# Optimization experiments

Hardware: AMD Instinct MI355X
Metric: run time of the kernel (lower is better)

The kernel has to match this reference:

```python
import jax, jax.numpy as jnp
import numpy as np

T, D, H, B = 2048, 1152, 16, 8
DH = D // H  # 72


def _apply_rope(x, cos_h, sin_h):
    # x: [T, H, DH]; cos_h, sin_h: [T, DH//2] (already chunked halves)
    c = jnp.concatenate([cos_h, cos_h], axis=-1)[:, None, :]  # [T,1,DH]
    s = jnp.concatenate([sin_h, sin_h], axis=-1)[:, None, :]
    x1, x2 = jnp.split(x, 2, axis=-1)
    rot = jnp.concatenate([-x2, x1], axis=-1)
    return x * c + rot * s


def setup_inputs() -> dict:
    key = jax.random.key(0)
    ks = jax.random.split(key, 12)
    hidden_states = jax.random.normal(ks[0], (T, D), jnp.float32)
    inner = jnp.sort(jax.random.randint(ks[1], (B - 1,), 1, T))
    cu_seqlens = jnp.concatenate(
        [jnp.zeros((1,), jnp.int32), inner.astype(jnp.int32), jnp.full((1,), T, jnp.int32)])
    cos = jax.random.uniform(ks[2], (T, DH), jnp.float32, -1.0, 1.0)
    sin = jax.random.uniform(ks[3], (T, DH), jnp.float32, -1.0, 1.0)
    std = 0.02
    Wq = jax.random.normal(ks[4], (D, D), jnp.float32) * std
    Wk = jax.random.normal(ks[5], (D, D), jnp.float32) * std
    Wv = jax.random.normal(ks[6], (D, D), jnp.float32) * std
    Wo = jax.random.normal(ks[7], (D, D), jnp.float32) * std
    bq = jnp.zeros((D,), jnp.float32)
    bk = jnp.zeros((D,), jnp.float32)
    bv = jnp.zeros((D,), jnp.float32)
    bo = jnp.zeros((D,), jnp.float32)
    return {"hidden_states": hidden_states, "cu_seqlens": cu_seqlens,
            "cos": cos, "sin": sin,
            "Wq": Wq, "bq": bq, "Wk": Wk, "bk": bk,
            "Wv": Wv, "bv": bv, "Wo": Wo, "bo": bo}


def reference(hidden_states, cu_seqlens, cos, sin, Wq, bq, Wk, bk, Wv, bv, Wo, bo):
    t = hidden_states.shape[0]
    scale = DH ** -0.5
    q = (hidden_states @ Wq.T + bq).reshape(t, H, DH)
    k = (hidden_states @ Wk.T + bk).reshape(t, H, DH)
    v = (hidden_states @ Wv.T + bv).reshape(t, H, DH)
    # RoPE: cos/sin [T, DH] are chunked in half along last dim, first half used
    cos_h = cos[:, : DH // 2]
    sin_h = sin[:, : DH // 2]
    q = _apply_rope(q, cos_h, sin_h)
    k = _apply_rope(k, cos_h, sin_h)
    # segment ids from cu_seqlens -> block-diagonal (varlen) attention mask
    pos = jnp.arange(t)
    seg = jnp.searchsorted(cu_seqlens, pos, side='right') - 1  # [T]
    mask = seg[:, None] == seg[None, :]  # [T, T]
    scores = jnp.einsum('thd,shd->hts', q, k) * scale  # [H, T, T]
    scores = jnp.where(mask[None], scores, jnp.float32(-1e30))
    attn = jax.nn.softmax(scores, axis=-1)
    out = jnp.einsum('hts,shd->thd', attn, v).reshape(t, D)
    return out @ Wo.T + bo
```

## Files before the change

kernel.cpp:

```cpp
#include <hip/hip_runtime.h>

#define TT 2048
#define DM 1152
#define NHEAD 16
#define HDIM 72
#define HDP 96
#define HDV 80
#define KSPLIT 2

typedef __attribute__((ext_vector_type(8))) __bf16 bf16x8;
typedef __attribute__((ext_vector_type(4))) float f32x4;
typedef unsigned short u16;
typedef unsigned int u32;

__device__ inline u16 f2bf(float f){
  u32 u = __builtin_bit_cast(u32, f);
  return (u16)((u + 0x7FFFu + ((u >> 16) & 1u)) >> 16);
}
__device__ inline float bf2f(u16 v){
  return __builtin_bit_cast(float, ((u32)v) << 16);
}
__device__ inline bf16x8 ldb8(const u16* p){
  uint4 u = *(const uint4*)p;
  return __builtin_bit_cast(bf16x8, u);
}
__device__ inline f32x4 mfma16(bf16x8 a, bf16x8 b, f32x4 c){
  return __builtin_amdgcn_mfma_f32_16x16x32_bf16(a, b, c, 0, 0, 0);
}
__device__ inline void gload_lds16(const u16* g, u16* l){
  __builtin_amdgcn_global_load_lds(
      (const __attribute__((address_space(1))) void*)g,
      (__attribute__((address_space(3))) void*)l, 16, 0, 0);
}

__global__ void k_convert(const float* hid, const float* wq, const float* wk,
                          const float* wv, const float* wo, const int* cu,
                          u16* hb, u16* wqb, u16* wkb, u16* wvb, u16* wob,
                          u16* qhb, u16* khb, int* seg)
{
  long i = (long)blockIdx.x * blockDim.x + threadIdx.x;
  const long NHID = (long)TT * DM;
  const long NW = (long)DM * DM;
  const long NCV = NHID + 4*NW;
  if (i < NHID) {
    hb[i] = f2bf(hid[i]);
  } else if (i < NCV) {
    long j = i - NHID;
    int w = (int)(j / NW);
    long o = j - (long)w * NW;
    const float* src = (w==0)?wq:(w==1)?wk:(w==2)?wv:wo;
    u16* dst = (w==0)?wqb:(w==1)?wkb:(w==2)?wvb:wob;
    dst[o] = f2bf(src[o]);
  } else {
    long j = i - NCV;
    const long PER = (long)NHEAD*TT*12;
    int arr = (int)(j / PER);
    long r = j - (long)arr*PER;
    long th = r / 12;
    int c = (int)(r - th*12);
    ((u32*)(arr ? khb : qhb))[th*48 + 36 + c] = 0u;
  }
  if (i < TT) {
    int c = 0;
    for (int e = 0; e < 9; ++e) c += (cu[e] <= (int)i);
    seg[i] = c - 1;
  }
}

__device__ __forceinline__ void gemm128_body(const u16* __restrict__ A,
                                             const u16* __restrict__ W,
                                             const float* __restrict__ bias,
                                             void* out, int mode, float oscale)
{
  __shared__ __align__(16) u16 As[128*32];
  __shared__ __align__(16) u16 Bs[128*32];
  int tid = threadIdx.x;
  int lane = tid & 63, wid = tid >> 6;
  int l15 = lane & 15, quad = lane >> 4;
  int bm = blockIdx.x * 128, bn = blockIdx.y * 128;
  int wm = (wid>>1)*64, wn = (wid&1)*64;
  f32x4 acc[4][4] = {};
  const u16* ga = A + (long)(bm + (tid>>2))*DM + (tid&3)*8;
  const u16* gb = W + (long)(bn + (tid>>2))*DM + (tid&3)*8;
  u16* lA = As + wid*512;
  u16* lB = Bs + wid*512;
  for (int k0 = 0; k0 < DM; k0 += 32) {
    gload_lds16(ga + k0,          lA);
    gload_lds16(ga + k0 + 64*DM,  lA + 2048);
    gload_lds16(gb + k0,          lB);
    gload_lds16(gb + k0 + 64*DM,  lB + 2048);
    __syncthreads();
    bf16x8 af[4], bfr[4];
    for (int i=0;i<4;i++) af[i]  = ldb8(As + (wm + i*16 + l15)*32 + quad*8);
    for (int i=0;i<4;i++) bfr[i] = ldb8(Bs + (wn + i*16 + l15)*32 + quad*8);
    for (int mi=0;mi<4;mi++)
      for (int ni=0;ni<4;ni++)
        acc[mi][ni] = mfma16(af[mi], bfr[ni], acc[mi][ni]);
    __syncthreads();
  }
  for (int ni=0;ni<4;ni++){
    int n = bn + wn + ni*16 + l15;
    float bv_ = bias[n];
    int h = n / HDIM, dh = n - (n / HDIM)*HDIM;
    for (int mi=0;mi<4;mi++){
      int m0 = bm + wm + mi*16 + quad*4;
      for (int r=0;r<4;r++){
        float v = (acc[mi][ni][r] + bv_) * oscale;
        int m = m0 + r;
        if (mode == 0) {
          ((u16*)out)[((long)(h*TT + m))*HDP + dh] = f2bf(v);
        } else {
          ((u16*)out)[((long)(h*HDV + dh))*TT + m] = f2bf(v);
        }
      }
    }
  }
}

__global__ __launch_bounds__(256) void k_gemm_qkv(const u16* __restrict__ A,
    const u16* __restrict__ Wq, const u16* __restrict__ Wk, const u16* __restrict__ Wv,
    const float* __restrict__ bq, const float* __restrict__ bk, const float* __restrict__ bv,
    u16* oq, u16* ok, u16* ov)
{
  const float scale = 0.11785113019775793f;
  int z = blockIdx.z;
  if (z == 0)      gemm128_body(A, Wq, bq, oq, 0, scale);
  else if (z == 1) gemm128_body(A, Wk, bk, ok, 0, 1.0f);
  else             gemm128_body(A, Wv, bv, ov, 2, 1.0f);
}

__global__ __launch_bounds__(256) void k_gemm_o(const u16* __restrict__ A,
    const u16* __restrict__ W, const float* __restrict__ bias, float* out)
{
  __shared__ __align__(16) u16 As[64*32];
  __shared__ __align__(16) u16 Bs[128*32];
  int tid = threadIdx.x;
  int lane = tid & 63, wid = tid >> 6;
  int l15 = lane & 15, quad = lane >> 4;
  int bm = blockIdx.x * 64, bn = blockIdx.y * 128;
  int wm = (wid>>1)*32, wn = (wid&1)*64;
  f32x4 acc[2][4] = {};
  const u16* ga = A + (long)(bm + (tid>>2))*DM + (tid&3)*8;
  const u16* gb = W + (long)(bn + (tid>>2))*DM + (tid&3)*8;
  u16* lA = As + wid*512;
  u16* lB = Bs + wid*512;
  for (int k0 = 0; k0 < DM; k0 += 32) {
    gload_lds16(ga + k0,          lA);
    gload_lds16(gb + k0,          lB);
    gload_lds16(gb + k0 + 64*DM,  lB + 2048);
    __syncthreads();
    bf16x8 af[2], bfr[4];
    for (int i=0;i<2;i++) af[i]  = ldb8(As + (wm + i*16 + l15)*32 + quad*8);
    for (int i=0;i<4;i++) bfr[i] = ldb8(Bs + (wn + i*16 + l15)*32 + quad*8);
    for (int mi=0;mi<2;mi++)
      for (int ni=0;ni<4;ni++)
        acc[mi][ni] = mfma16(af[mi], bfr[ni], acc[mi][ni]);
    __syncthreads();
  }
  for (int ni=0;ni<4;ni++){
    int n = bn + wn + ni*16 + l15;
    float bv_ = bias[n];
    for (int mi=0;mi<2;mi++){
      int m0 = bm + wm + mi*16 + quad*4;
      for (int r=0;r<4;r++)
        out[(long)(m0 + r)*DM + n] = acc[mi][ni][r] + bv_;
    }
  }
}

__global__ void k_rope(u16* qh, u16* kh, const float* __restrict__ cosb,
                       const float* __restrict__ sinb)
{
  int i = blockIdx.x * blockDim.x + threadIdx.x;
  const int total = 2 * NHEAD * TT * 36;
  if (i >= total) return;
  int d = i % 36; int rest = i / 36;
  int t = rest % TT; rest /= TT;
  int h = rest % NHEAD; int qk = rest / NHEAD;
  u16* base = (qk ? kh : qh) + ((long)h*TT + t)*HDP;
  float x1 = bf2f(base[d]), x2 = bf2f(base[d+36]);
  float c = cosb[t*HDIM + d], s = sinb[t*HDIM + d];
  base[d]    = f2bf(x1*c - x2*s);
  base[d+36] = f2bf(x2*c + x1*s);
}

__global__ __launch_bounds__(256) void k_attn(const u16* __restrict__ qh,
                                              const u16* __restrict__ kh,
                                              const u16* __restrict__ vT,
                                              const int* __restrict__ seg,
                                              const int* __restrict__ cu,
                                              float* __restrict__ pacc,
                                              float* __restrict__ plsum)
{
  __shared__ __align__(16) u16 Ks[2][64*96];
  __shared__ __align__(16) u16 pbuf[4][16][72];
  int h = blockIdx.y;
  int z = blockIdx.z;
  int tid = threadIdx.x, lane = tid & 63, wid = tid >> 6;
  int l15 = lane & 15, quad = lane >> 4;
  int qb0 = blockIdx.x * 64;
  int qbase = qb0 + wid*16;

  const u16* qp = qh + ((long)h*TT + qbase + l15)*HDP + quad*8;
  bf16x8 qf0 = ldb8(qp), qf1 = ldb8(qp+32), qf2 = ldb8(qp+64);
  int segq[4];
  for (int r=0;r<4;r++) segq[r] = seg[qbase + quad*4 + r];
  f32x4 acc[5] = {};
  float lsum[4] = {0.f, 0.f, 0.f, 0.f};

  int seg_lo = seg[qb0], seg_hi = seg[qb0 + 63];
  int s_begin = cu[seg_lo] & ~63;
  int s_end = cu[seg_hi + 1];
  int nt = (s_end - s_begin + 63) >> 6;
  int nt0 = (nt + 1) >> 1;
  int it_lo = z ? nt0 : 0;
  int it_hi = z ? nt : nt0;

  const u16* kbase = kh + (long)h*TT*HDP;

  if (it_lo < it_hi) {
    {
      const u16* gk = kbase + (long)(s_begin + it_lo*64)*HDP + tid*8;
      u16* lK = Ks[0] + wid*512;
      gload_lds16(gk,        lK);
      gload_lds16(gk + 2048, lK + 2048);
      gload_lds16(gk + 4096, lK + 4096);
    }
    for (int it = it_lo; it < it_hi; ++it) {
      int s0 = s_begin + it*64;
      int cur = (it - it_lo) & 1;
      __syncthreads();
      if (it + 1 < it_hi) {
        const u16* gk = kbase + (long)(s0 + 64)*HDP + tid*8;
        u16* lK = Ks[cur^1] + wid*512;
        gload_lds16(gk,        lK);
        gload_lds16(gk + 2048, lK + 2048);
        gload_lds16(gk + 4096, lK + 4096);
      }
      f32x4 sc[4] = {};
      for (int j=0;j<4;j++){
        const u16* kp = Ks[cur] + (j*16 + l15)*96 + quad*8;
        sc[j] = mfma16(qf0, ldb8(kp),    sc[j]);
        sc[j] = mfma16(qf1, ldb8(kp+32), sc[j]);
        sc[j] = mfma16(qf2, ldb8(kp+64), sc[j]);
      }
      int sg[4];
      for (int j=0;j<4;j++) sg[j] = seg[s0 + j*16 + l15];
      float p[4][4];
      for (int j=0;j<4;j++)
        for (int r=0;r<4;r++){
          p[j][r] = (sg[j] == segq[r]) ? __expf(sc[j][r]) : 0.f;
          lsum[r] += p[j][r];
        }
      for (int j=0;j<4;j++)
        for (int r=0;r<4;r++)
          pbuf[wid][quad*4+r][j*16+l15] = f2bf(p[j][r]);
      bf16x8 pf0 = ldb8(&pbuf[wid][l15][quad*8]);
      bf16x8 pf1 = ldb8(&pbuf[wid][l15][32 + quad*8]);
      const u16* vp = vT + ((long)h*HDV + l15)*TT + s0 + quad*8;
      for (int n=0;n<5;n++){
        bf16x8 vf0 = ldb8(vp + (long)n*16*TT);
        bf16x8 vf1 = ldb8(vp + (long)n*16*TT + 32);
        acc[n] = mfma16(pf0, vf0, acc[n]);
        acc[n] = mfma16(pf1, vf1, acc[n]);
      }
    }
  }
  for (int off=1; off<16; off<<=1)
    for (int r=0;r<4;r++)
      lsum[r] += __shfl_xor(lsum[r], off, 64);
  for (int n=0;n<5;n++){
    int dh = n*16 + l15;
    for (int r=0;r<4;r++){
      int t = qbase + quad*4 + r;
      pacc[(((long)z*TT + t)*NHEAD + h)*HDV + dh] = acc[n][r];
    }
  }
  if (l15 == 0){
    for (int r=0;r<4;r++){
      int t = qbase + quad*4 + r;
      plsum[((long)z*TT + t)*NHEAD + h] = lsum[r];
    }
  }
}

__global__ void k_combine(const float* __restrict__ pacc,
                          const float* __restrict__ plsum,
                          u16* __restrict__ ao)
{
  int i = blockIdx.x*blockDim.x + threadIdx.x;
  const int total = TT*NHEAD*HDIM;
  if (i >= total) return;
  int dh = i % HDIM; int rest = i / HDIM;
  int h = rest % NHEAD; int t = rest / NHEAD;
  long i0 = ((long)t*NHEAD + h)*HDV + dh;
  float a = pacc[i0] + pacc[(long)TT*NHEAD*HDV + i0];
  float l = plsum[t*NHEAD + h] + plsum[TT*NHEAD + t*NHEAD + h];
  ao[(long)t*DM + h*HDIM + dh] = f2bf(a / l);
}

extern "C" void kernel_launch(void* const* d_in, const int* in_sizes, int n_in,
                              void* d_out, int out_size, void* d_ws, size_t ws_size,
                              hipStream_t stream)
{
  const float* hid  = (const float*)d_in[0];
  const int*   cu   = (const int*)d_in[1];
  const float* cosb = (const float*)d_in[2];
  const float* sinb = (const float*)d_in[3];
  const float* wq   = (const float*)d_in[4];
  const float* bq   = (const float*)d_in[5];
  const float* wk   = (const float*)d_in[6];
  const float* bk   = (const float*)d_in[7];
  const float* wv   = (const float*)d_in[8];
  const float* bv   = (const float*)d_in[9];
  const float* wo   = (const float*)d_in[10];
  const float* bo   = (const float*)d_in[11];

  char* ws = (char*)d_ws;
  u16* hb  = (u16*)ws; ws += (long)TT*DM*2;
  u16* wqb = (u16*)ws; ws += (long)DM*DM*2;
  u16* wkb = (u16*)ws; ws += (long)DM*DM*2;
  u16* wvb = (u16*)ws; ws += (long)DM*DM*2;
  u16* wob = (u16*)ws; ws += (long)DM*DM*2;
  u16* qhb = (u16*)ws; ws += (long)NHEAD*TT*HDP*2;
  u16* khb = (u16*)ws; ws += (long)NHEAD*TT*HDP*2;
  u16* vTb = (u16*)ws; ws += (long)NHEAD*HDV*TT*2;
  u16* aob = (u16*)ws; ws += (long)TT*DM*2;
  int* seg = (int*)ws; ws += (long)TT*4;
  float* pacc  = (float*)ws; ws += (long)KSPLIT*TT*NHEAD*HDV*4;
  float* plsum = (float*)ws; ws += (long)KSPLIT*TT*NHEAD*4;

  long nconv = (long)TT*DM + 4L*DM*DM + 2L*NHEAD*TT*12;
  k_convert<<<dim3((nconv + 255)/256), 256, 0, stream>>>(
      hid, wq, wk, wv, wo, cu, hb, wqb, wkb, wvb, wob, qhb, khb, seg);

  dim3 gqkv(TT/128, DM/128, 3);
  k_gemm_qkv<<<gqkv, 256, 0, stream>>>(hb, wqb, wkb, wvb, bq, bk, bv, qhb, khb, vTb);

  int nrope = 2*NHEAD*TT*36;
  k_rope<<<dim3((nrope + 255)/256), 256, 0, stream>>>(qhb, khb, cosb, sinb);

  dim3 ga(TT/64, NHEAD, KSPLIT);
  k_attn<<<ga, 256, 0, stream>>>(qhb, khb, vTb, seg, cu, pacc, plsum);

  int ncomb = TT*NHEAD*HDIM;
  k_combine<<<dim3((ncomb + 255)/256), 256, 0, stream>>>(pacc, plsum, aob);

  dim3 go(TT/64, DM/128);
  k_gemm_o<<<go, 256, 0, stream>>>(aob, wob, bo, (float*)d_out);
}
```

Before: 205.4 us.

## Double-buffer GEMMs with smaller tiles, vectorize conversion, range-based attention mask

The QKV and output-projection GEMMs now use double-buffered LDS with a single barrier per k-step. Their N tile is halved to 64, which roughly doubles the block count and improves occupancy on the many CUs, and launch bounds request 4 blocks per CU. The fp32-to-bf16 conversion kernel is vectorized to handle four elements per thread. The attention mask now compares key indices against per-row segment bounds instead of loading segment ids for every key tile. Smaller tiles lower per-block data reuse and raise the total number of global loads.

```diff
diff --git a/kernel.cpp b/kernel.cpp
--- a/kernel.cpp
+++ b/kernel.cpp
@@ -12,6 +12,7 @@
 typedef __attribute__((ext_vector_type(4))) float f32x4;
 typedef unsigned short u16;
 typedef unsigned int u32;
+typedef __attribute__((ext_vector_type(4))) u16 u16x4;
 
 __device__ inline u16 f2bf(float f){
   u32 u = __builtin_bit_cast(u32, f);
@@ -39,26 +40,32 @@
                           u16* qhb, u16* khb, int* seg)
 {
   long i = (long)blockIdx.x * blockDim.x + threadIdx.x;
-  const long NHID = (long)TT * DM;
-  const long NW = (long)DM * DM;
-  const long NCV = NHID + 4*NW;
-  if (i < NHID) {
-    hb[i] = f2bf(hid[i]);
-  } else if (i < NCV) {
-    long j = i - NHID;
-    int w = (int)(j / NW);
-    long o = j - (long)w * NW;
-    const float* src = (w==0)?wq:(w==1)?wk:(w==2)?wv:wo;
-    u16* dst = (w==0)?wqb:(w==1)?wkb:(w==2)?wvb:wob;
-    dst[o] = f2bf(src[o]);
+  const long NHID4 = (long)TT * DM / 4;
+  const long NW4 = (long)DM * DM / 4;
+  const long NC4 = NHID4 + 4*NW4;
+  if (i < NC4) {
+    const float4* src; u16* dst; long o;
+    if (i < NHID4) { src = (const float4*)hid; dst = hb; o = i; }
+    else {
+      long j = i - NHID4;
+      int w = (int)(j / NW4);
+      o = j - (long)w * NW4;
+      src = (const float4*)((w==0)?wq:(w==1)?wk:(w==2)?wv:wo);
+      dst = (w==0)?wqb:(w==1)?wkb:(w==2)?wvb:wob;
+    }
+    float4 v = src[o];
+    u16x4 r; r.x = f2bf(v.x); r.y = f2bf(v.y); r.z = f2bf(v.z); r.w = f2bf(v.w);
+    *(u16x4*)(dst + o*4) = r;
   } else {
-    long j = i - NCV;
+    long j = i - NC4;
     const long PER = (long)NHEAD*TT*12;
-    int arr = (int)(j / PER);
-    long r = j - (long)arr*PER;
-    long th = r / 12;
-    int c = (int)(r - th*12);
-    ((u32*)(arr ? khb : qhb))[th*48 + 36 + c] = 0u;
+    if (j < 2*PER) {
+      int arr = (int)(j / PER);
+      long r = j - (long)arr*PER;
+      long th = r / 12;
+      int c = (int)(r - th*12);
+      ((u32*)(arr ? khb : qhb))[th*48 + 36 + c] = 0u;
+    }
   }
   if (i < TT) {
     int c = 0;
@@ -67,42 +74,48 @@
   }
 }
 
-__device__ __forceinline__ void gemm128_body(const u16* __restrict__ A,
+__device__ __forceinline__ void gemm_m128n64(const u16* __restrict__ A,
                                              const u16* __restrict__ W,
                                              const float* __restrict__ bias,
                                              void* out, int mode, float oscale)
 {
-  __shared__ __align__(16) u16 As[128*32];
-  __shared__ __align__(16) u16 Bs[128*32];
+  __shared__ __align__(16) u16 As[2][128*32];
+  __shared__ __align__(16) u16 Bs[2][64*32];
   int tid = threadIdx.x;
   int lane = tid & 63, wid = tid >> 6;
   int l15 = lane & 15, quad = lane >> 4;
-  int bm = blockIdx.x * 128, bn = blockIdx.y * 128;
-  int wm = (wid>>1)*64, wn = (wid&1)*64;
-  f32x4 acc[4][4] = {};
+  int bm = blockIdx.x * 128, bn = blockIdx.y * 64;
+  int wm = wid*32;
+  f32x4 acc[2][4] = {};
   const u16* ga = A + (long)(bm + (tid>>2))*DM + (tid&3)*8;
   const u16* gb = W + (long)(bn + (tid>>2))*DM + (tid&3)*8;
-  u16* lA = As + wid*512;
-  u16* lB = Bs + wid*512;
-  for (int k0 = 0; k0 < DM; k0 += 32) {
-    gload_lds16(ga + k0,          lA);
-    gload_lds16(ga + k0 + 64*DM,  lA + 2048);
-    gload_lds16(gb + k0,          lB);
-    gload_lds16(gb + k0 + 64*DM,  lB + 2048);
+  {
+    u16* lA = As[0] + wid*512; u16* lB = Bs[0] + wid*512;
+    gload_lds16(ga,          lA);
+    gload_lds16(ga + 64*DM,  lA + 2048);
+    gload_lds16(gb,          lB);
+  }
+  int cur = 0;
+  for (int k0 = 0; k0 < DM; k0 += 32, cur ^= 1) {
     __syncthreads();
-    bf16x8 af[4], bfr[4];
-    for (int i=0;i<4;i++) af[i]  = ldb8(As + (wm + i*16 + l15)*32 + quad*8);
-    for (int i=0;i<4;i++) bfr[i] = ldb8(Bs + (wn + i*16 + l15)*32 + quad*8);
-    for (int mi=0;mi<4;mi++)
+    if (k0 + 32 < DM) {
+      u16* lA = As[cur^1] + wid*512; u16* lB = Bs[cur^1] + wid*512;
+      gload_lds16(ga + k0 + 32,          lA);
+      gload_lds16(ga + k0 + 32 + 64*DM,  lA + 2048);
+      gload_lds16(gb + k0 + 32,          lB);
+    }
+    bf16x8 af[2], bfr[4];
+    for (int i=0;i<2;i++) af[i]  = ldb8(As[cur] + (wm + i*16 + l15)*32 + quad*8);
+    for (int i=0;i<4;i++) bfr[i] = ldb8(Bs[cur] + (i*16 + l15)*32 + quad*8);
+    for (int mi=0;mi<2;mi++)
       for (int ni=0;ni<4;ni++)
         acc[mi][ni] = mfma16(af[mi], bfr[ni], acc[mi][ni]);
-    __syncthreads();
   }
   for (int ni=0;ni<4;ni++){
-    int n = bn + wn + ni*16 + l15;
+    int n = bn + ni*16 + l15;
     float bv_ = bias[n];
     int h = n / HDIM, dh = n - (n / HDIM)*HDIM;
-    for (int mi=0;mi<4;mi++){
+    for (int mi=0;mi<2;mi++){
       int m0 = bm + wm + mi*16 + quad*4;
       for (int r=0;r<4;r++){
         float v = (acc[mi][ni][r] + bv_) * oscale;
@@ -117,47 +130,50 @@
   }
 }
 
-__global__ __launch_bounds__(256) void k_gemm_qkv(const u16* __restrict__ A,
+__global__ __launch_bounds__(256, 4) void k_gemm_qkv(const u16* __restrict__ A,
     const u16* __restrict__ Wq, const u16* __restrict__ Wk, const u16* __restrict__ Wv,
     const float* __restrict__ bq, const float* __restrict__ bk, const float* __restrict__ bv,
     u16* oq, u16* ok, u16* ov)
 {
   const float scale = 0.11785113019775793f;
   int z = blockIdx.z;
-  if (z == 0)      gemm128_body(A, Wq, bq, oq, 0, scale);
-  else if (z == 1) gemm128_body(A, Wk, bk, ok, 0, 1.0f);
-  else             gemm128_body(A, Wv, bv, ov, 2, 1.0f);
-}
-
-__global__ __launch_bounds__(256) void k_gemm_o(const u16* __restrict__ A,
+  if (z == 0)      gemm_m128n64(A, Wq, bq, oq, 0, scale);
+  else if (z == 1) gemm_m128n64(A, Wk, bk, ok, 0, 1.0f);
+  else             gemm_m128n64(A, Wv, bv, ov, 2, 1.0f);
+}
+
+__global__ __launch_bounds__(256, 4) void k_gemm_o(const u16* __restrict__ A,
     const u16* __restrict__ W, const float* __restrict__ bias, float* out)
 {
-  __shared__ __align__(16) u16 As[64*32];
-  __shared__ __align__(16) u16 Bs[128*32];
+  __shared__ __align__(16) u16 As[2][64*32];
+  __shared__ __align__(16) u16 Bs[2][64*32];
   int tid = threadIdx.x;
   int lane = tid & 63, wid = tid >> 6;
   int l15 = lane & 15, quad = lane >> 4;
-  int bm = blockIdx.x * 64, bn = blockIdx.y * 128;
-  int wm = (wid>>1)*32, wn = (wid&1)*64;
-  f32x4 acc[2][4] = {};
+  int bm = blockIdx.x * 64, bn = blockIdx.y * 64;
+  int wm = (wid>>1)*32, wn = (wid&1)*32;
+  f32x4 acc[2][2] = {};
   const u16* ga = A + (long)(bm + (tid>>2))*DM + (tid&3)*8;
   const u16* gb = W + (long)(bn + (tid>>2))*DM + (tid&3)*8;
-  u16* lA = As + wid*512;
-  u16* lB = Bs + wid*512;
-  for (int k0 = 0; k0 < DM; k0 += 32) {
-    gload_lds16(ga + k0,          lA);
-    gload_lds16(gb + k0,          lB);
-    gload_lds16(gb + k0 + 64*DM,  lB + 2048);
+  {
+    gload_lds16(ga, As[0] + wid*512);
+    gload_lds16(gb, Bs[0] + wid*512);
+  }
+  int cur = 0;
+  for (int k0 = 0; k0 < DM; k0 += 32, cur ^= 1) {
     __syncthreads();
-    bf16x8 af[2], bfr[4];
-    for (int i=0;i<2;i++) af[i]  = ldb8(As + (wm + i*16 + l15)*32 + quad*8);
-    for (int i=0;i<4;i++) bfr[i] = ldb8(Bs + (wn + i*16 + l15)*32 + quad*8);
+    if (k0 + 32 < DM) {
+      gload_lds16(ga + k0 + 32, As[cur^1] + wid*512);
+      gload_lds16(gb + k0 + 32, Bs[cur^1] + wid*512);
+    }
+    bf16x8 af[2], bfr[2];
+    for (int i=0;i<2;i++) af[i]  = ldb8(As[cur] + (wm + i*16 + l15)*32 + quad*8);
+    for (int i=0;i<2;i++) bfr[i] = ldb8(Bs[cur] + (wn + i*16 + l15)*32 + quad*8);
     for (int mi=0;mi<2;mi++)
-      for (int ni=0;ni<4;ni++)
+      for (int ni=0;ni<2;ni++)
         acc[mi][ni] = mfma16(af[mi], bfr[ni], acc[mi][ni]);
-    __syncthreads();
-  }
-  for (int ni=0;ni<4;ni++){
+  }
+  for (int ni=0;ni<2;ni++){
     int n = bn + wn + ni*16 + l15;
     float bv_ = bias[n];
     for (int mi=0;mi<2;mi++){
@@ -203,20 +219,23 @@
 
   const u16* qp = qh + ((long)h*TT + qbase + l15)*HDP + quad*8;
   bf16x8 qf0 = ldb8(qp), qf1 = ldb8(qp+32), qf2 = ldb8(qp+64);
-  int segq[4];
-  for (int r=0;r<4;r++) segq[r] = seg[qbase + quad*4 + r];
+  int lo[4], hi[4];
+  for (int r=0;r<4;r++){
+    int sq = seg[qbase + quad*4 + r];
+    lo[r] = cu[sq]; hi[r] = cu[sq+1];
+  }
   f32x4 acc[5] = {};
   float lsum[4] = {0.f, 0.f, 0.f, 0.f};
 
-  int seg_lo = seg[qb0], seg_hi = seg[qb0 + 63];
-  int s_begin = cu[seg_lo] & ~63;
-  int s_end = cu[seg_hi + 1];
+  int s_begin = cu[seg[qb0]] & ~63;
+  int s_end = cu[seg[qb0 + 63] + 1];
   int nt = (s_end - s_begin + 63) >> 6;
   int nt0 = (nt + 1) >> 1;
   int it_lo = z ? nt0 : 0;
   int it_hi = z ? nt : nt0;
 
   const u16* kbase = kh + (long)h*TT*HDP;
+  const u16* vbase = vT + ((long)h*HDV + l15)*TT + quad*8;
 
   if (it_lo < it_hi) {
     {
@@ -244,20 +263,21 @@
         sc[j] = mfma16(qf1, ldb8(kp+32), sc[j]);
         sc[j] = mfma16(qf2, ldb8(kp+64), sc[j]);
       }
-      int sg[4];
-      for (int j=0;j<4;j++) sg[j] = seg[s0 + j*16 + l15];
       float p[4][4];
-      for (int j=0;j<4;j++)
+      for (int j=0;j<4;j++){
+        int kidx = s0 + j*16 + l15;
         for (int r=0;r<4;r++){
-          p[j][r] = (sg[j] == segq[r]) ? __expf(sc[j][r]) : 0.f;
+          bool in = (kidx >= lo[r]) && (kidx < hi[r]);
+          p[j][r] = in ? __expf(sc[j][r]) : 0.f;
           lsum[r] += p[j][r];
         }
+      }
       for (int j=0;j<4;j++)
         for (int r=0;r<4;r++)
           pbuf[wid][quad*4+r][j*16+l15] = f2bf(p[j][r]);
       bf16x8 pf0 = ldb8(&pbuf[wid][l15][quad*8]);
       bf16x8 pf1 = ldb8(&pbuf[wid][l15][32 + quad*8]);
-      const u16* vp = vT + ((long)h*HDV + l15)*TT + s0 + quad*8;
+      const u16* vp = vbase + s0;
       for (int n=0;n<5;n++){
         bf16x8 vf0 = ldb8(vp + (long)n*16*TT);
         bf16x8 vf1 = ldb8(vp + (long)n*16*TT + 32);
@@ -330,11 +350,11 @@
   float* pacc  = (float*)ws; ws += (long)KSPLIT*TT*NHEAD*HDV*4;
   float* plsum = (float*)ws; ws += (long)KSPLIT*TT*NHEAD*4;
 
-  long nconv = (long)TT*DM + 4L*DM*DM + 2L*NHEAD*TT*12;
+  long nconv = ((long)TT*DM + 4L*DM*DM)/4 + 2L*NHEAD*TT*12;
   k_convert<<<dim3((nconv + 255)/256), 256, 0, stream>>>(
       hid, wq, wk, wv, wo, cu, hb, wqb, wkb, wvb, wob, qhb, khb, seg);
 
-  dim3 gqkv(TT/128, DM/128, 3);
+  dim3 gqkv(TT/128, DM/64, 3);
   k_gemm_qkv<<<gqkv, 256, 0, stream>>>(hb, wqb, wkb, wvb, bq, bk, bv, qhb, khb, vTb);
 
   int nrope = 2*NHEAD*TT*36;
@@ -346,6 +366,6 @@
   int ncomb = TT*NHEAD*HDIM;
   k_combine<<<dim3((ncomb + 255)/256), 256, 0, stream>>>(pacc, plsum, aob);
 
-  dim3 go(TT/64, DM/128);
+  dim3 go(TT/64, DM/64);
   k_gemm_o<<<go, 256, 0, stream>>>(aob, wob, bo, (float*)d_out);
 }
```

Measured after the change: 203.2 us. No clear change (-1.1%).
